# Kernel tuning notes

Hardware: AMD Instinct MI355X
Metric: run time of the kernel (lower is better)

Reference implementation:

```python
import jax, jax.numpy as jnp
import numpy as np

TAU = 0.01
MASK_VALUE = -1000000.0


def setup_inputs() -> dict:
    key = jax.random.key(0)
    kq, kk, km, k1, k2, k3 = jax.random.split(key, 6)
    B, Lq, Lk = 4, 512, 512
    Dq = Dk = 256
    H = 128
    queries = jax.random.normal(kq, (B, Lq, Dq), dtype=jnp.float32)
    keys = jax.random.normal(kk, (B, Lk, Dk), dtype=jnp.float32)
    # valid length along the size-2 logits axis, in {1, 2}
    mask = jax.random.randint(km, (B, Lq, Lk), 1, 3, dtype=jnp.int32)
    Wq = jax.random.normal(k1, (H, Dq), dtype=jnp.float32) * 0.05
    Wk = jax.random.normal(k2, (H, Dk), dtype=jnp.float32) * 0.05
    Wv = jax.random.normal(k3, (2, H), dtype=jnp.float32) * 0.05
    return {"queries": queries, "keys": keys, "mask": mask,
            "Wq": Wq, "Wk": Wk, "Wv": Wv}


def reference(queries, keys, mask, Wq, Wk, Wv):
    # Linear projections (no bias): [B,Lq,H], [B,Lk,H]
    q = jnp.einsum('bqd,hd->bqh', queries, Wq)
    k = jnp.einsum('bkd,hd->bkh', keys, Wk)
    # Bahdanau broadcast-add + tanh: [B,Lq,Lk,H]
    features = jnp.tanh(q[:, :, None, :] + k[:, None, :, :])
    # Project to 2 logits: [B,Lq,Lk,2]
    scores = jnp.einsum('bqkh,ch->bqkc', features, Wv)
    # sequence_mask along the size-2 last axis: positions >= valid_len get -1e6
    pos = jnp.arange(2, dtype=mask.dtype)
    masked = jnp.where(pos < mask[..., None], scores, MASK_VALUE)
    # Gumbel-softmax (soft), tau=0.01, over last axis; take channel 0
    g = jax.random.gumbel(jax.random.key(42), masked.shape, dtype=masked.dtype)
    weights = jax.nn.softmax((masked + g) / TAU, axis=-1)
    return weights[..., 0]
```

## Files before the change

### kernel.cpp

```cpp
#include <hip/hip_runtime.h>
#include <stdint.h>


#define BB 4
#define LLEN 512
#define DD 256
#define HH 128

#define TWO_LOG2E 2.8853900817779268f
#define LOG2E_100 144.26950408889634f

__device__ __forceinline__ uint32_t rotl32(uint32_t v, int r) {
  return (v << r) | (v >> (32 - r));
}

__device__ __forceinline__ void tf2x32(uint32_t x0, uint32_t x1,
                                       uint32_t& o0, uint32_t& o1) {
  const uint32_t k0 = 0u;
  const uint32_t k1 = 42u;
  const uint32_t k2 = 0x1BD11BDAu ^ k0 ^ k1;

  x0 += k0; x1 += k1;
#define TFR(r) { x0 += x1; x1 = rotl32(x1, (r)); x1 ^= x0; }
  TFR(13) TFR(15) TFR(26) TFR(6)
  x0 += k1; x1 += k2 + 1u;
  TFR(17) TFR(29) TFR(16) TFR(24)
  x0 += k2; x1 += k0 + 2u;
  TFR(13) TFR(15) TFR(26) TFR(6)
  x0 += k0; x1 += k1 + 3u;
  TFR(17) TFR(29) TFR(16) TFR(24)
  x0 += k1; x1 += k2 + 4u;
  TFR(13) TFR(15) TFR(26) TFR(6)
  x0 += k2; x1 += k0 + 5u;
#undef TFR
  o0 = x0; o1 = x1;
}

__device__ __forceinline__ float jax_u01(uint32_t flat) {
  uint32_t o0, o1;
  tf2x32(0u, flat, o0, o1);
  const uint32_t bits = o0 ^ o1;
  const float f = __uint_as_float((bits >> 9) | 0x3F800000u) - 1.0f;
  return fmaxf(f, 1.17549435e-38f);
}

__global__ __launch_bounds__(128) void proj_kernel(
    const float* __restrict__ queries, const float* __restrict__ keys,
    const float* __restrict__ Wq, const float* __restrict__ Wk,
    float* __restrict__ EQ, float* __restrict__ EK) {
  const int blk = blockIdx.x;
  const bool isK = blk >= 512;
  const int rb = (isK ? blk - 512 : blk) * 4;
  const float* __restrict__ in = isK ? keys : queries;
  const float* __restrict__ W  = isK ? Wk : Wq;
  float* __restrict__ outp     = isK ? EK : EQ;

  __shared__ float rows[4][DD];
  const float4* in4 = reinterpret_cast<const float4*>(in + (size_t)rb * DD);
  float4* rows4 = reinterpret_cast<float4*>(&rows[0][0]);
  #pragma unroll
  for (int t = threadIdx.x; t < 4 * DD / 4; t += 128) rows4[t] = in4[t];
  __syncthreads();

  const int h = threadIdx.x;
  const float4* W4 = reinterpret_cast<const float4*>(W + (size_t)h * DD);
  float a0 = 0.f, a1 = 0.f, a2 = 0.f, a3 = 0.f;
  #pragma unroll 8
  for (int d4 = 0; d4 < DD / 4; ++d4) {
    const float4 w = W4[d4];
    const int d = d4 * 4;
    a0 = fmaf(w.x, rows[0][d], fmaf(w.y, rows[0][d+1], fmaf(w.z, rows[0][d+2], fmaf(w.w, rows[0][d+3], a0))));
    a1 = fmaf(w.x, rows[1][d], fmaf(w.y, rows[1][d+1], fmaf(w.z, rows[1][d+2], fmaf(w.w, rows[1][d+3], a1))));
    a2 = fmaf(w.x, rows[2][d], fmaf(w.y, rows[2][d+1], fmaf(w.z, rows[2][d+2], fmaf(w.w, rows[2][d+3], a2))));
    a3 = fmaf(w.x, rows[3][d], fmaf(w.y, rows[3][d+1], fmaf(w.z, rows[3][d+2], fmaf(w.w, rows[3][d+3], a3))));
  }
  float* orow = outp + (size_t)rb * HH + h;
  orow[0 * HH] = __builtin_amdgcn_exp2f(a0 * TWO_LOG2E);
  orow[1 * HH] = __builtin_amdgcn_exp2f(a1 * TWO_LOG2E);
  orow[2 * HH] = __builtin_amdgcn_exp2f(a2 * TWO_LOG2E);
  orow[3 * HH] = __builtin_amdgcn_exp2f(a3 * TWO_LOG2E);
}


#define GRP(accv, qv, kv, wd) {                                       \
    float4 A_;                                                        \
    A_.x = fmaf((qv).x, (kv).x, 1.0f);                                \
    A_.y = fmaf((qv).y, (kv).y, 1.0f);                                \
    A_.z = fmaf((qv).z, (kv).z, 1.0f);                                \
    A_.w = fmaf((qv).w, (kv).w, 1.0f);                                \
    const float p01_ = A_.x * A_.y;                                   \
    const float p23_ = A_.z * A_.w;                                   \
    const float n01_ = fmaf((wd).x, A_.y, (wd).y * A_.x);             \
    const float n23_ = fmaf((wd).z, A_.w, (wd).w * A_.z);             \
    const float num_ = fmaf(n01_, p23_, n23_ * p01_);                 \
    const float rc_  = __builtin_amdgcn_rcpf(p01_ * p23_);            \
    (accv) = fmaf(num_, rc_, (accv)); }

__global__ __launch_bounds__(256) void attn_kernel(
    const float* __restrict__ EQ, const float* __restrict__ EK,
    const int* __restrict__ mask, const float* __restrict__ Wv,
    float* __restrict__ out) {
  __shared__ float4 QL[16][33];
  __shared__ float4 KL[64][33];
  __shared__ float4 wdL[32];

  const int bi = blockIdx.x, bj = blockIdx.y, b = blockIdx.z;
  const int i0 = bi * 16, j0 = bj * 64;

  const float4* Q4 = reinterpret_cast<const float4*>(EQ) + ((size_t)b * LLEN + i0) * (HH / 4);
  const float4* K4 = reinterpret_cast<const float4*>(EK) + ((size_t)b * LLEN + j0) * (HH / 4);
  for (int t = threadIdx.x; t < 512 + 2048; t += 256) {
    if (t < 512) {
      QL[t >> 5][t & 31] = Q4[t];
    } else {
      const int u = t - 512;
      KL[u >> 5][u & 31] = K4[u];
    }
  }
  if (threadIdx.x < 32) {
    const float4 w0 = reinterpret_cast<const float4*>(Wv)[threadIdx.x];
    const float4 w1 = reinterpret_cast<const float4*>(Wv)[32 + threadIdx.x];
    float4 wd; wd.x = w0.x - w1.x; wd.y = w0.y - w1.y;
    wd.z = w0.z - w1.z; wd.w = w0.w - w1.w;
    wdL[threadIdx.x] = wd;
  }
  __syncthreads();

  const int jj = threadIdx.x & 31;
  const int ib = threadIdx.x >> 5;

  const uint32_t row0 = (uint32_t)b * LLEN + i0 + ib;
  const uint32_t col0 = j0 + jj;
  const uint32_t idx00 = row0 * LLEN + col0;
  const uint32_t idx01 = idx00 + 32u;
  const uint32_t idx10 = idx00 + 8u * LLEN;
  const uint32_t idx11 = idx10 + 32u;
  const int m00 = mask[idx00], m01 = mask[idx01];
  const int m10 = mask[idx10], m11 = mask[idx11];

  float Swd = 0.f;
  #pragma unroll
  for (int t = 0; t < 32; ++t) {
    const float4 wd = wdL[t];
    Swd += (wd.x + wd.y) + (wd.z + wd.w);
  }

  float acc00 = 0.f, acc01 = 0.f, acc10 = 0.f, acc11 = 0.f;

  #pragma unroll 4
  for (int h4 = 0; h4 < HH / 4; ++h4) {
    const float4 kv0 = KL[jj][h4];
    const float4 kv1 = KL[jj + 32][h4];
    const float4 qv0 = QL[ib][h4];
    const float4 qv1 = QL[ib + 8][h4];
    const float4 wd  = wdL[h4];
    GRP(acc00, qv0, kv0, wd)
    GRP(acc01, qv0, kv1, wd)
    GRP(acc10, qv1, kv0, wd)
    GRP(acc11, qv1, kv1, wd)
  }

  #define EPI(accv, mreg, idx) {                                        \
      float o_ = 1.0f;                                                  \
      if ((mreg) >= 2) {                                                \
        const float d_  = fmaf(-2.0f, (accv), Swd);                     \
        const float l0_ = __log2f(jax_u01((idx) * 2u));                 \
        const float l1_ = __log2f(jax_u01((idx) * 2u + 1u));            \
        const float rl_ = l1_ * __builtin_amdgcn_rcpf(l0_);             \
        const float dl_ = __log2f(rl_);                                 \
        const float t_  = fmaf(d_, LOG2E_100, 100.0f * dl_);            \
        o_ = __builtin_amdgcn_rcpf(1.0f + __builtin_amdgcn_exp2f(-t_)); \
      }                                                                 \
      out[idx] = o_; }

  EPI(acc00, m00, idx00)
  EPI(acc01, m01, idx01)
  EPI(acc10, m10, idx10)
  EPI(acc11, m11, idx11)
  #undef EPI
}

extern "C" void kernel_launch(void* const* d_in, const int* in_sizes, int n_in,
                              void* d_out, int out_size, void* d_ws, size_t ws_size,
                              hipStream_t stream) {
  const float* queries = (const float*)d_in[0];
  const float* keys    = (const float*)d_in[1];
  const int*   mask    = (const int*)d_in[2];
  const float* Wq      = (const float*)d_in[3];
  const float* Wk      = (const float*)d_in[4];
  const float* Wv      = (const float*)d_in[5];
  float* out = (float*)d_out;

  float* EQ = (float*)d_ws;
  float* EK = EQ + (size_t)BB * LLEN * HH;

  proj_kernel<<<dim3(1024), dim3(128), 0, stream>>>(
      queries, keys, Wq, Wk, EQ, EK);
  attn_kernel<<<dim3(LLEN / 16, LLEN / 64, BB), dim3(256), 0, stream>>>(
      EQ, EK, mask, Wv, out);
}
```

Measured before the change: 46.70 us.

## Split attention kernel into compute loop and separate Gumbel epilogue kernel

Splits the fused attention kernel into two launches. The first computes the tanh-projection accumulators and writes the score differences to a workspace buffer. The second reads those differences and the mask, runs the Threefry Gumbel noise and sigmoid, and writes the output. The epilogue is now branch-free, computing noise for every element and selecting by mask. The aim is lower register pressure and no divergence in each kernel, at the cost of an extra launch, an extra global round trip of 1M floats, and noise work on masked elements.

After: 49.14 us. +5.2%, slower.

```diff
diff --git a/kernel.cpp b/kernel.cpp
--- a/kernel.cpp
+++ b/kernel.cpp
@@ -81,7 +81,6 @@
   orow[3 * HH] = __builtin_amdgcn_exp2f(a3 * TWO_LOG2E);
 }
 
-
 #define GRP(accv, qv, kv, wd) {                                       \
     float4 A_;                                                        \
     A_.x = fmaf((qv).x, (kv).x, 1.0f);                                \
@@ -96,10 +95,9 @@
     const float rc_  = __builtin_amdgcn_rcpf(p01_ * p23_);            \
     (accv) = fmaf(num_, rc_, (accv)); }
 
-__global__ __launch_bounds__(256) void attn_kernel(
+__global__ __launch_bounds__(256) void attn_loop(
     const float* __restrict__ EQ, const float* __restrict__ EK,
-    const int* __restrict__ mask, const float* __restrict__ Wv,
-    float* __restrict__ out) {
+    const float* __restrict__ Wv, float* __restrict__ dbuf) {
   __shared__ float4 QL[16][33];
   __shared__ float4 KL[64][33];
   __shared__ float4 wdL[32];
@@ -128,15 +126,6 @@
 
   const int jj = threadIdx.x & 31;
   const int ib = threadIdx.x >> 5;
-
-  const uint32_t row0 = (uint32_t)b * LLEN + i0 + ib;
-  const uint32_t col0 = j0 + jj;
-  const uint32_t idx00 = row0 * LLEN + col0;
-  const uint32_t idx01 = idx00 + 32u;
-  const uint32_t idx10 = idx00 + 8u * LLEN;
-  const uint32_t idx11 = idx10 + 32u;
-  const int m00 = mask[idx00], m01 = mask[idx01];
-  const int m10 = mask[idx10], m11 = mask[idx11];
 
   float Swd = 0.f;
   #pragma unroll
@@ -160,23 +149,51 @@
     GRP(acc11, qv1, kv1, wd)
   }
 
-  #define EPI(accv, mreg, idx) {                                        \
-      float o_ = 1.0f;                                                  \
-      if ((mreg) >= 2) {                                                \
-        const float d_  = fmaf(-2.0f, (accv), Swd);                     \
-        const float l0_ = __log2f(jax_u01((idx) * 2u));                 \
-        const float l1_ = __log2f(jax_u01((idx) * 2u + 1u));            \
-        const float rl_ = l1_ * __builtin_amdgcn_rcpf(l0_);             \
-        const float dl_ = __log2f(rl_);                                 \
-        const float t_  = fmaf(d_, LOG2E_100, 100.0f * dl_);            \
-        o_ = __builtin_amdgcn_rcpf(1.0f + __builtin_amdgcn_exp2f(-t_)); \
-      }                                                                 \
-      out[idx] = o_; }
-
-  EPI(acc00, m00, idx00)
-  EPI(acc01, m01, idx01)
-  EPI(acc10, m10, idx10)
-  EPI(acc11, m11, idx11)
+  const uint32_t tg = (((uint32_t)blockIdx.z * gridDim.y + blockIdx.y) * gridDim.x
+                       + blockIdx.x) * 256u + threadIdx.x;
+  float4 v;
+  v.x = fmaf(-2.0f, acc00, Swd);
+  v.y = fmaf(-2.0f, acc01, Swd);
+  v.z = fmaf(-2.0f, acc10, Swd);
+  v.w = fmaf(-2.0f, acc11, Swd);
+  reinterpret_cast<float4*>(dbuf)[tg] = v;
+}
+
+__global__ __launch_bounds__(256) void attn_epi(
+    const float* __restrict__ dbuf, const int* __restrict__ mask,
+    float* __restrict__ out) {
+  const int bi = blockIdx.x, bj = blockIdx.y, b = blockIdx.z;
+  const int i0 = bi * 16, j0 = bj * 64;
+  const int jj = threadIdx.x & 31;
+  const int ib = threadIdx.x >> 5;
+
+  const uint32_t tg = (((uint32_t)blockIdx.z * gridDim.y + blockIdx.y) * gridDim.x
+                       + blockIdx.x) * 256u + threadIdx.x;
+  const float4 d4 = reinterpret_cast<const float4*>(dbuf)[tg];
+
+  const uint32_t row0 = (uint32_t)b * LLEN + i0 + ib;
+  const uint32_t col0 = j0 + jj;
+  const uint32_t idx00 = row0 * LLEN + col0;
+  const uint32_t idx01 = idx00 + 32u;
+  const uint32_t idx10 = idx00 + 8u * LLEN;
+  const uint32_t idx11 = idx10 + 32u;
+
+  const int m00 = mask[idx00], m01 = mask[idx01];
+  const int m10 = mask[idx10], m11 = mask[idx11];
+
+  #define EPI(dv, mreg, idx) {                                          \
+      const float l0_ = __log2f(jax_u01((idx) * 2u));                   \
+      const float l1_ = __log2f(jax_u01((idx) * 2u + 1u));              \
+      const float rl_ = l1_ * __builtin_amdgcn_rcpf(l0_);               \
+      const float dl_ = __log2f(rl_);                                   \
+      const float t_  = fmaf((dv), LOG2E_100, 100.0f * dl_);            \
+      const float oc_ = __builtin_amdgcn_rcpf(1.0f + __builtin_amdgcn_exp2f(-t_)); \
+      out[idx] = ((mreg) >= 2) ? oc_ : 1.0f; }
+
+  EPI(d4.x, m00, idx00)
+  EPI(d4.y, m01, idx01)
+  EPI(d4.z, m10, idx10)
+  EPI(d4.w, m11, idx11)
   #undef EPI
 }
 
@@ -191,11 +208,14 @@
   const float* Wv      = (const float*)d_in[5];
   float* out = (float*)d_out;
 
-  float* EQ = (float*)d_ws;
-  float* EK = EQ + (size_t)BB * LLEN * HH;
+  float* EQ   = (float*)d_ws;
+  float* EK   = EQ + (size_t)BB * LLEN * HH;
+  float* dbuf = EK + (size_t)BB * LLEN * HH;
 
   proj_kernel<<<dim3(1024), dim3(128), 0, stream>>>(
       queries, keys, Wq, Wk, EQ, EK);
-  attn_kernel<<<dim3(LLEN / 16, LLEN / 64, BB), dim3(256), 0, stream>>>(
-      EQ, EK, mask, Wv, out);
-}
+  attn_loop<<<dim3(LLEN / 16, LLEN / 64, BB), dim3(256), 0, stream>>>(
+      EQ, EK, Wv, dbuf);
+  attn_epi<<<dim3(LLEN / 16, LLEN / 64, BB), dim3(256), 0, stream>>>(
+      dbuf, mask, out);
+}
```

## Split Gumbel epilogue into compacted second kernel and enlarge query tile

Applied to the files above, without the earlier changes.

The attention kernel now computes 32 query rows per block (8 outputs per thread) and, instead of running the expensive Threefry/log epilogue divergently, ballot-compacts masked entries per wave into a workspace buffer with their score difference. A new kernel then processes the compacted entries densely, so all lanes do useful Gumbel work. Rotates use alignbit. This adds an extra launch and workspace traffic in exchange for removing wave divergence in the epilogue, and the larger tile raises register pressure.

After: 47.22 us. No clear change (+1.1%).

```diff
diff --git a/kernel.cpp b/kernel.cpp
--- a/kernel.cpp
+++ b/kernel.cpp
@@ -10,8 +10,11 @@
 #define TWO_LOG2E 2.8853900817779268f
 #define LOG2E_100 144.26950408889634f
 
+#define NWAVES 2048
+#define REGION 512
+
 __device__ __forceinline__ uint32_t rotl32(uint32_t v, int r) {
-  return (v << r) | (v >> (32 - r));
+  return __builtin_amdgcn_alignbit(v, v, 32 - r);
 }
 
 __device__ __forceinline__ void tf2x32(uint32_t x0, uint32_t x1,
@@ -81,7 +84,6 @@
   orow[3 * HH] = __builtin_amdgcn_exp2f(a3 * TWO_LOG2E);
 }
 
-
 #define GRP(accv, qv, kv, wd) {                                       \
     float4 A_;                                                        \
     A_.x = fmaf((qv).x, (kv).x, 1.0f);                                \
@@ -96,24 +98,25 @@
     const float rc_  = __builtin_amdgcn_rcpf(p01_ * p23_);            \
     (accv) = fmaf(num_, rc_, (accv)); }
 
-__global__ __launch_bounds__(256) void attn_kernel(
+__global__ __launch_bounds__(256) void attn_loop(
     const float* __restrict__ EQ, const float* __restrict__ EK,
     const int* __restrict__ mask, const float* __restrict__ Wv,
-    float* __restrict__ out) {
-  __shared__ float4 QL[16][33];
+    float* __restrict__ out, uint32_t* __restrict__ counts,
+    uint2* __restrict__ entbuf) {
+  __shared__ float4 QL[32][33];
   __shared__ float4 KL[64][33];
   __shared__ float4 wdL[32];
 
   const int bi = blockIdx.x, bj = blockIdx.y, b = blockIdx.z;
-  const int i0 = bi * 16, j0 = bj * 64;
+  const int i0 = bi * 32, j0 = bj * 64;
 
   const float4* Q4 = reinterpret_cast<const float4*>(EQ) + ((size_t)b * LLEN + i0) * (HH / 4);
   const float4* K4 = reinterpret_cast<const float4*>(EK) + ((size_t)b * LLEN + j0) * (HH / 4);
-  for (int t = threadIdx.x; t < 512 + 2048; t += 256) {
-    if (t < 512) {
+  for (int t = threadIdx.x; t < 1024 + 2048; t += 256) {
+    if (t < 1024) {
       QL[t >> 5][t & 31] = Q4[t];
     } else {
-      const int u = t - 512;
+      const int u = t - 1024;
       KL[u >> 5][u & 31] = K4[u];
     }
   }
@@ -131,12 +134,12 @@
 
   const uint32_t row0 = (uint32_t)b * LLEN + i0 + ib;
   const uint32_t col0 = j0 + jj;
-  const uint32_t idx00 = row0 * LLEN + col0;
-  const uint32_t idx01 = idx00 + 32u;
-  const uint32_t idx10 = idx00 + 8u * LLEN;
-  const uint32_t idx11 = idx10 + 32u;
-  const int m00 = mask[idx00], m01 = mask[idx01];
-  const int m10 = mask[idx10], m11 = mask[idx11];
+  int mreg[4][2];
+  #pragma unroll
+  for (int r = 0; r < 4; ++r)
+    #pragma unroll
+    for (int c = 0; c < 2; ++c)
+      mreg[r][c] = mask[(row0 + 8u * r) * LLEN + col0 + 32u * c];
 
   float Swd = 0.f;
   #pragma unroll
@@ -145,39 +148,79 @@
     Swd += (wd.x + wd.y) + (wd.z + wd.w);
   }
 
-  float acc00 = 0.f, acc01 = 0.f, acc10 = 0.f, acc11 = 0.f;
+  float acc[4][2] = {{0.f,0.f},{0.f,0.f},{0.f,0.f},{0.f,0.f}};
 
   #pragma unroll 4
   for (int h4 = 0; h4 < HH / 4; ++h4) {
     const float4 kv0 = KL[jj][h4];
     const float4 kv1 = KL[jj + 32][h4];
+    const float4 wd  = wdL[h4];
     const float4 qv0 = QL[ib][h4];
     const float4 qv1 = QL[ib + 8][h4];
-    const float4 wd  = wdL[h4];
-    GRP(acc00, qv0, kv0, wd)
-    GRP(acc01, qv0, kv1, wd)
-    GRP(acc10, qv1, kv0, wd)
-    GRP(acc11, qv1, kv1, wd)
-  }
-
-  #define EPI(accv, mreg, idx) {                                        \
-      float o_ = 1.0f;                                                  \
-      if ((mreg) >= 2) {                                                \
-        const float d_  = fmaf(-2.0f, (accv), Swd);                     \
-        const float l0_ = __log2f(jax_u01((idx) * 2u));                 \
-        const float l1_ = __log2f(jax_u01((idx) * 2u + 1u));            \
-        const float rl_ = l1_ * __builtin_amdgcn_rcpf(l0_);             \
-        const float dl_ = __log2f(rl_);                                 \
-        const float t_  = fmaf(d_, LOG2E_100, 100.0f * dl_);            \
-        o_ = __builtin_amdgcn_rcpf(1.0f + __builtin_amdgcn_exp2f(-t_)); \
-      }                                                                 \
-      out[idx] = o_; }
-
-  EPI(acc00, m00, idx00)
-  EPI(acc01, m01, idx01)
-  EPI(acc10, m10, idx10)
-  EPI(acc11, m11, idx11)
-  #undef EPI
+    const float4 qv2 = QL[ib + 16][h4];
+    const float4 qv3 = QL[ib + 24][h4];
+    GRP(acc[0][0], qv0, kv0, wd) GRP(acc[0][1], qv0, kv1, wd)
+    GRP(acc[1][0], qv1, kv0, wd) GRP(acc[1][1], qv1, kv1, wd)
+    GRP(acc[2][0], qv2, kv0, wd) GRP(acc[2][1], qv2, kv1, wd)
+    GRP(acc[3][0], qv3, kv0, wd) GRP(acc[3][1], qv3, kv1, wd)
+  }
+
+  const int lane = threadIdx.x & 63;
+  const unsigned long long lanemask_lt = (1ull << lane) - 1ull;
+  const uint32_t wave_id =
+      (((uint32_t)blockIdx.z * gridDim.y + blockIdx.y) * gridDim.x + blockIdx.x) * 4u
+      + (threadIdx.x >> 6);
+  uint2* __restrict__ reg = entbuf + (size_t)wave_id * REGION;
+
+  uint32_t off = 0;
+  #pragma unroll
+  for (int r = 0; r < 4; ++r) {
+    #pragma unroll
+    for (int c = 0; c < 2; ++c) {
+      const uint32_t idx = (row0 + 8u * r) * LLEN + col0 + 32u * c;
+      const bool need = (mreg[r][c] >= 2);
+      const unsigned long long bal = __ballot(need);
+      if (need) {
+        const uint32_t rank = (uint32_t)__popcll(bal & lanemask_lt);
+        uint2 ent;
+        ent.x = idx;
+        ent.y = __float_as_uint(fmaf(-2.0f, acc[r][c], Swd));
+        reg[off + rank] = ent;
+      } else {
+        out[idx] = 1.0f;
+      }
+      off += (uint32_t)__popcll(bal);
+    }
+  }
+  if (lane == 0) counts[wave_id] = off;
+}
+
+__global__ __launch_bounds__(256) void attn_epi(
+    const uint32_t* __restrict__ counts, const uint2* __restrict__ entbuf,
+    float* __restrict__ out) {
+  const int lane = threadIdx.x & 63;
+  const uint32_t g = (uint32_t)blockIdx.x * 4u + (threadIdx.x >> 6);
+  const uint32_t cnt = counts[g];
+  if (cnt == 0) return;
+  const uint2* __restrict__ reg = entbuf + (size_t)g * REGION;
+
+  const int iters = (int)((cnt + 63u) >> 6);
+  #pragma unroll 2
+  for (int k = 0; k < iters; ++k) {
+    const uint32_t e = (uint32_t)k * 64u + (uint32_t)lane;
+    const bool valid = e < cnt;
+    const uint32_t eL = valid ? e : (cnt - 1u);
+    const uint2 ent = reg[eL];
+
+    const float dv = __uint_as_float(ent.y);
+    const float l0 = __log2f(jax_u01(ent.x * 2u));
+    const float l1 = __log2f(jax_u01(ent.x * 2u + 1u));
+    const float rl = l1 * __builtin_amdgcn_rcpf(l0);
+    const float dl = __log2f(rl);
+    const float t  = fmaf(dv, LOG2E_100, 100.0f * dl);
+    const float o  = __builtin_amdgcn_rcpf(1.0f + __builtin_amdgcn_exp2f(-t));
+    if (valid) out[ent.x] = o;
+  }
 }
 
 extern "C" void kernel_launch(void* const* d_in, const int* in_sizes, int n_in,
@@ -193,9 +236,13 @@
 
   float* EQ = (float*)d_ws;
   float* EK = EQ + (size_t)BB * LLEN * HH;
+  uint32_t* counts = (uint32_t*)(EK + (size_t)BB * LLEN * HH);
+  uint2* entbuf = (uint2*)((char*)counts + 16384);
 
   proj_kernel<<<dim3(1024), dim3(128), 0, stream>>>(
       queries, keys, Wq, Wk, EQ, EK);
-  attn_kernel<<<dim3(LLEN / 16, LLEN / 64, BB), dim3(256), 0, stream>>>(
-      EQ, EK, mask, Wv, out);
-}
+  attn_loop<<<dim3(LLEN / 32, LLEN / 64, BB), dim3(256), 0, stream>>>(
+      EQ, EK, mask, Wv, out, counts, entbuf);
+  attn_epi<<<dim3(NWAVES / 4), dim3(256), 0, stream>>>(
+      counts, entbuf, out);
+}
```
